# Optimization experiments

Hardware: AMD Instinct MI355X
Metric: run time of the kernel (lower is better)

The kernel has to match this reference:

```python
import jax, jax.numpy as jnp
import numpy as np

B, T, D_MODEL, N_HEADS, N_KV = 2, 2048, 1024, 16, 4
HEAD = D_MODEL // N_HEADS  # 64
NEG_INF = -1e9


def sine_table(features, length):
    # standard RoPE frequency table: theta_i = 10000^(2i/d)
    fraction = jnp.arange(0, features, 2, dtype=jnp.float32) / features
    timescale = 10000.0 ** fraction  # (features/2,)
    sinusoid = jnp.arange(length, dtype=jnp.float32)[:, None] / timescale[None, :]
    sinusoid = jnp.concatenate([sinusoid, sinusoid], axis=-1)  # (L, features)
    return jnp.sin(sinusoid), jnp.cos(sinusoid)


def rotate_half(x):
    x1, x2 = jnp.split(x, 2, axis=-1)
    return jnp.concatenate([-x2, x1], axis=-1)


def apply_rope(x, sin, cos):
    # x: (B, H, T, D); sin/cos: (L, D)
    t = x.shape[-2]
    return x * cos[:t][None, None] + rotate_half(x) * sin[:t][None, None]


def setup_inputs() -> dict:
    key = jax.random.key(0)
    k1, k2, k3, k4 = jax.random.split(key, 4)
    return {
        'q': jax.random.normal(k1, (B, T, D_MODEL), dtype=jnp.float32),
        'k': jax.random.normal(k2, (B, T, N_KV * HEAD), dtype=jnp.float32),
        'v': jax.random.normal(k3, (B, T, N_KV * HEAD), dtype=jnp.float32),
        'w_out': jax.random.normal(k4, (D_MODEL, D_MODEL), dtype=jnp.float32) * 0.02,
    }


def reference(q, k, v, w_out):
    Bq, Tq, C = q.shape
    head = C // N_HEADS
    # split heads: q -> (B, n_heads, T, head); k/v -> (B, n_kv, T, head)
    qh = q.reshape(Bq, Tq, N_HEADS, head).transpose(0, 2, 1, 3)
    kh = k.reshape(Bq, Tq, N_KV, head).transpose(0, 2, 1, 3)
    vh = v.reshape(Bq, Tq, N_KV, head).transpose(0, 2, 1, 3)
    # inline RoPE on q and k
    sin, cos = sine_table(head, Tq)
    qh = apply_rope(qh, sin, cos)
    kh = apply_rope(kh, sin, cos)
    # GQA repeat of kv heads to match q heads
    rep = N_HEADS // N_KV
    kh = jnp.repeat(kh, rep, axis=1)
    vh = jnp.repeat(vh, rep, axis=1)
    # manual scaled-dot-product attention with causal masking (full T^2 logits)
    logits = jnp.einsum('bhqd,bhkd->bhqk', qh, kh) / jnp.sqrt(jnp.float32(head))
    causal = jnp.tril(jnp.ones((Tq, Tq), dtype=jnp.float32))
    logits = jnp.where(causal == 0, NEG_INF, logits)
    attn = jax.nn.softmax(logits, axis=-1)
    out = jnp.einsum('bhqk,bhkd->bhqd', attn, vh)
    out = out.transpose(0, 2, 1, 3).reshape(Bq, Tq, C)
    return out @ w_out
```

## Files before the change

kernel.cpp:

```cpp
#include <hip/hip_runtime.h>
#include <math.h>

#define T_SEQ 2048
#define NH    16
#define NKV   4

typedef __attribute__((ext_vector_type(8)))  _Float16 f16x8;
typedef __attribute__((ext_vector_type(4)))  _Float16 f16x4;
typedef __attribute__((ext_vector_type(2)))  __fp16   fp16x2b;
typedef __attribute__((ext_vector_type(4)))  float    f32x4;

#if __has_builtin(__builtin_amdgcn_exp2f)
#define EXP2F(x) __builtin_amdgcn_exp2f(x)
#else
#define EXP2F(x) exp2f(x)
#endif

#define QSCALE 0.18033688011112042f

__global__ __launch_bounds__(256) void prep_kernel(const float* __restrict__ k,
                                                   const float* __restrict__ v,
                                                   const float* __restrict__ w,
                                                   float2* __restrict__ tb,
                                                   _Float16* __restrict__ Kr,
                                                   _Float16* __restrict__ Vt,
                                                   _Float16* __restrict__ Wt)
{
    __shared__ _Float16 L[64 * 72];
    const int bx = blockIdx.x;
    if (bx < 256) {
        int idx = bx * 256 + threadIdx.x;
        int i = idx & 31, t = idx >> 5;
        float inv = __expf((float)i * (-9.210340371976184f / 32.0f));
        float ang = (float)t * inv;
        tb[idx] = make_float2(cosf(ang), sinf(ang));
    } else if (bx < 512) {
        int idx = (bx - 256) * 256 + threadIdx.x;
        int i   = idx & 31;
        int t   = idx >> 5;
        float inv = __expf((float)i * (-9.210340371976184f / 32.0f));
        float ang = (float)t * inv;
        float sn = sinf(ang), cs = cosf(ang);
        #pragma unroll
        for (int bk = 0; bk < 8; ++bk) {
            const float* src = k + ((size_t)(bk >> 2) * T_SEQ + t) * 256 + (bk & 3) * 64 + i;
            float x1 = src[0], x2 = src[32];
            _Float16* dst = Kr + ((size_t)bk * T_SEQ + t) * 64 + i;
            dst[0]  = (_Float16)(x1 * cs - x2 * sn);
            dst[32] = (_Float16)(x2 * cs + x1 * sn);
        }
    } else if (bx < 768) {
        const int id = bx - 512;
        const int t0 = (id & 31) * 64, bk = id >> 5;
        const int b = bk >> 2, kh = bk & 3;
        const int rr = threadIdx.x >> 2, pp = threadIdx.x & 3;
        const float* src = v + ((size_t)(b * T_SEQ + t0 + rr)) * 256 + kh * 64 + pp * 16;
        f32x4 s0 = *(const f32x4*)(src), s1 = *(const f32x4*)(src + 4);
        f32x4 s2 = *(const f32x4*)(src + 8), s3 = *(const f32x4*)(src + 12);
        _Float16* lp = &L[rr * 72 + pp * 16];
        #pragma unroll
        for (int j = 0; j < 4; ++j) { lp[j] = (_Float16)s0[j]; lp[4+j] = (_Float16)s1[j];
                                      lp[8+j] = (_Float16)s2[j]; lp[12+j] = (_Float16)s3[j]; }
        __syncthreads();
        f16x8 w0, w1;
        #pragma unroll
        for (int j = 0; j < 8; ++j) w0[j] = L[(pp * 16 + j) * 72 + rr];
        #pragma unroll
        for (int j = 0; j < 8; ++j) w1[j] = L[(pp * 16 + 8 + j) * 72 + rr];
        _Float16* dst = Vt + ((size_t)bk * 64 + rr) * T_SEQ + t0 + pp * 16;
        *(f16x8*)dst = w0; *(f16x8*)(dst + 8) = w1;
    } else {
        const int id = bx - 768;
        const int k0 = (id & 15) * 64, n0 = (id >> 4) * 64;
        const int rr = threadIdx.x >> 2, pp = threadIdx.x & 3;
        const float* src = w + (size_t)(k0 + rr) * 1024 + n0 + pp * 16;
        f32x4 s0 = *(const f32x4*)(src), s1 = *(const f32x4*)(src + 4);
        f32x4 s2 = *(const f32x4*)(src + 8), s3 = *(const f32x4*)(src + 12);
        _Float16* lp = &L[rr * 72 + pp * 16];
        #pragma unroll
        for (int j = 0; j < 4; ++j) { lp[j] = (_Float16)s0[j]; lp[4+j] = (_Float16)s1[j];
                                      lp[8+j] = (_Float16)s2[j]; lp[12+j] = (_Float16)s3[j]; }
        __syncthreads();
        f16x8 w0, w1;
        #pragma unroll
        for (int j = 0; j < 8; ++j) w0[j] = L[(pp * 16 + j) * 72 + rr];
        #pragma unroll
        for (int j = 0; j < 8; ++j) w1[j] = L[(pp * 16 + 8 + j) * 72 + rr];
        _Float16* dst = Wt + (size_t)(n0 + rr) * 1024 + k0 + pp * 16;
        *(f16x8*)dst = w0; *(f16x8*)(dst + 8) = w1;
    }
}


__global__ __launch_bounds__(256) void attn_kernel(const float* __restrict__ q,
                                                   const float2* __restrict__ tb,
                                                   const _Float16* __restrict__ Kr,
                                                   const _Float16* __restrict__ Vt,
                                                   _Float16* __restrict__ AO)
{
    __shared__ _Float16 smem[16384];

    const int wid  = threadIdx.x >> 6;
    const int lane = threadIdx.x & 63;
    const int bh = blockIdx.x & 31;
    const int pp = blockIdx.x >> 5;
    const int p  = (pp < 8) ? pp : (23 - pp);
    const int qb0 = p, qb1 = 31 - p;
    const int b = bh >> 4, h = bh & 15;
    const int kh = h >> 2;
    const int bkh = b * NKV + kh;
    const int g = lane >> 4, r = lane & 15;

    const int srow   = wid * 16 + (lane >> 3);
    const int schunk = lane & 7;
    const _Float16* kgbase = Kr + (size_t)bkh * T_SEQ * 64;
    const _Float16* vgbase = Vt + (size_t)bkh * 64 * T_SEQ;
    const int kd0 = srow * 64 + ((schunk ^ (srow & 7)) * 8);
    const int kd1 = kd0 + 8 * 64;

    f16x8 stK0, stK1, stV0, stV1;
    {
        const _Float16* kg = kgbase + (size_t)srow * 64 + schunk * 8;
        stK0 = *(const f16x8*)(kg);
        stK1 = *(const f16x8*)(kg + 8 * 64);
        const _Float16* vg = vgbase + (size_t)srow * T_SEQ + schunk * 8;
        stV0 = *(const f16x8*)(vg);
        stV1 = *(const f16x8*)(vg + 8 * T_SEQ);
    }

    f16x8 qa[2][2];
    #pragma unroll
    for (int tl = 0; tl < 2; ++tl) {
        const int t = (tl ? qb1 : qb0) * 64 + wid * 16 + r;
        const float* qs = q + ((size_t)b * T_SEQ + t) * 1024 + h * 64 + 8 * g;
        const float2* tp = tb + t * 32 + 8 * g;
        #pragma unroll
        for (int j = 0; j < 8; ++j) {
            float x0 = qs[j], x1 = qs[32 + j];
            float2 cs = tp[j];
            qa[tl][0][j] = (_Float16)((x0 * cs.x - x1 * cs.y) * QSCALE);
            qa[tl][1][j] = (_Float16)((x1 * cs.x + x0 * cs.y) * QSCALE);
        }
    }

    *(f16x8*)(&smem[kd0])        = stK0;
    *(f16x8*)(&smem[kd1])        = stK1;
    *(f16x8*)(&smem[8192 + kd0]) = stV0;
    *(f16x8*)(&smem[8192 + kd1]) = stV1;
    __syncthreads();

    f32x4 o[2][4];
    f32x4 o4[2];
    #pragma unroll
    for (int tl = 0; tl < 2; ++tl) {
        #pragma unroll
        for (int db = 0; db < 4; ++db) o[tl][db] = (f32x4){0.f,0.f,0.f,0.f};
        o4[tl] = (f32x4){0.f,0.f,0.f,0.f};
    }
    const f16x4 onesf = {(_Float16)1.f, (_Float16)1.f, (_Float16)1.f, (_Float16)1.f};
    float mrun[2] = {-INFINITY, -INFINITY};
    int cur = 0;

    for (int kvb = 0; kvb <= qb1; ++kvb) {
        const bool hasNext = (kvb < qb1);
        if (hasNext) {
            const int nb = (kvb + 1) * 64;
            const _Float16* kg = kgbase + (size_t)(nb + srow) * 64 + schunk * 8;
            stK0 = *(const f16x8*)(kg);
            stK1 = *(const f16x8*)(kg + 8 * 64);
            const _Float16* vg = vgbase + (size_t)srow * T_SEQ + nb + schunk * 8;
            stV0 = *(const f16x8*)(vg);
            stV1 = *(const f16x8*)(vg + 8 * T_SEQ);
        }
        const bool act0 = (kvb <= qb0);
        const _Float16* ks = smem + cur * 4096;
        const _Float16* vs = smem + 8192 + cur * 4096;

        f32x4 stt[2][4];
        __builtin_amdgcn_s_setprio(1);
        #pragma unroll
        for (int kt = 0; kt < 4; ++kt) {
            f16x8 ka0 = *(const f16x8*)(ks + (kt*16 + r) * 64 + ((g       ^ (r & 7)) * 8));
            f16x8 ka1 = *(const f16x8*)(ks + (kt*16 + r) * 64 + (((4 + g) ^ (r & 7)) * 8));
            f32x4 s1 = {0.f,0.f,0.f,0.f};
            s1 = __builtin_amdgcn_mfma_f32_16x16x32_f16(ka0, qa[1][0], s1, 0, 0, 0);
            s1 = __builtin_amdgcn_mfma_f32_16x16x32_f16(ka1, qa[1][1], s1, 0, 0, 0);
            stt[1][kt] = s1;
            if (act0) {
                f32x4 s0 = {0.f,0.f,0.f,0.f};
                s0 = __builtin_amdgcn_mfma_f32_16x16x32_f16(ka0, qa[0][0], s0, 0, 0, 0);
                s0 = __builtin_amdgcn_mfma_f32_16x16x32_f16(ka1, qa[0][1], s0, 0, 0, 0);
                stt[0][kt] = s0;
            }
        }
        __builtin_amdgcn_s_setprio(0);

        if (kvb == qb0) {
            #pragma unroll
            for (int kt = 0; kt < 4; ++kt)
                #pragma unroll
                for (int j = 0; j < 4; ++j)
                    if (kt*16 + 4*g + j > wid*16 + r) stt[0][kt][j] = -1e9f;
        }
        if (kvb == qb1) {
            #pragma unroll
            for (int kt = 0; kt < 4; ++kt)
                #pragma unroll
                for (int j = 0; j < 4; ++j)
                    if (kt*16 + 4*g + j > wid*16 + r) stt[1][kt][j] = -1e9f;
        }

        f16x4 pf[2][4];
        #pragma unroll
        for (int tl = 0; tl < 2; ++tl) {
            if (tl == 0 && !act0) continue;
            float a0 = fmaxf(fmaxf(stt[tl][0][0], stt[tl][0][1]),
                             fmaxf(stt[tl][0][2], stt[tl][0][3]));
            float a1 = fmaxf(fmaxf(stt[tl][1][0], stt[tl][1][1]),
                             fmaxf(stt[tl][1][2], stt[tl][1][3]));
            float a2 = fmaxf(fmaxf(stt[tl][2][0], stt[tl][2][1]),
                             fmaxf(stt[tl][2][2], stt[tl][2][3]));
            float a3 = fmaxf(fmaxf(stt[tl][3][0], stt[tl][3][1]),
                             fmaxf(stt[tl][3][2], stt[tl][3][3]));
            float pmL = fmaxf(fmaxf(a0, a1), fmaxf(a2, a3));
            if (!__all(pmL <= mrun[tl] + 8.0f)) {
                float pm = fmaxf(pmL, __shfl_xor(pmL, 16));
                pm = fmaxf(pm, __shfl_xor(pm, 32));
                float mn   = fmaxf(mrun[tl], pm);
                float corr = EXP2F(mrun[tl] - mn);
                mrun[tl]   = mn;
                f32x4 cf = { __shfl(corr, 4*g + 0), __shfl(corr, 4*g + 1),
                             __shfl(corr, 4*g + 2), __shfl(corr, 4*g + 3) };
                o[tl][0] *= cf; o[tl][1] *= cf; o[tl][2] *= cf; o[tl][3] *= cf;
                o4[tl]   *= cf;
            }
            #pragma unroll
            for (int kt = 0; kt < 4; ++kt) {
                float p0 = EXP2F(stt[tl][kt][0] - mrun[tl]);
                float p1 = EXP2F(stt[tl][kt][1] - mrun[tl]);
                float p2 = EXP2F(stt[tl][kt][2] - mrun[tl]);
                float p3 = EXP2F(stt[tl][kt][3] - mrun[tl]);
                union { unsigned u[2]; f16x4 v; } pk;
                union { fp16x2b hh; unsigned u; } c0, c1;
                c0.hh = __builtin_amdgcn_cvt_pkrtz(p0, p1);
                c1.hh = __builtin_amdgcn_cvt_pkrtz(p2, p3);
                pk.u[0] = c0.u; pk.u[1] = c1.u;
                pf[tl][kt] = pk.v;
            }
        }

        __builtin_amdgcn_s_setprio(1);
        #pragma unroll
        for (int kt = 0; kt < 4; ++kt) {
            const int vc = ((2*kt + (g >> 1)) ^ (r & 7)) * 8 + (g & 1) * 4;
            f16x4 v0 = *(const f16x4*)(vs + (0*16 + r) * 64 + vc);
            f16x4 v1 = *(const f16x4*)(vs + (1*16 + r) * 64 + vc);
            f16x4 v2 = *(const f16x4*)(vs + (2*16 + r) * 64 + vc);
            f16x4 v3 = *(const f16x4*)(vs + (3*16 + r) * 64 + vc);
            o[1][0] = __builtin_amdgcn_mfma_f32_16x16x16f16(pf[1][kt], v0, o[1][0], 0, 0, 0);
            o[1][1] = __builtin_amdgcn_mfma_f32_16x16x16f16(pf[1][kt], v1, o[1][1], 0, 0, 0);
            o[1][2] = __builtin_amdgcn_mfma_f32_16x16x16f16(pf[1][kt], v2, o[1][2], 0, 0, 0);
            o[1][3] = __builtin_amdgcn_mfma_f32_16x16x16f16(pf[1][kt], v3, o[1][3], 0, 0, 0);
            o4[1]   = __builtin_amdgcn_mfma_f32_16x16x16f16(pf[1][kt], onesf, o4[1], 0, 0, 0);
            if (act0) {
                o[0][0] = __builtin_amdgcn_mfma_f32_16x16x16f16(pf[0][kt], v0, o[0][0], 0, 0, 0);
                o[0][1] = __builtin_amdgcn_mfma_f32_16x16x16f16(pf[0][kt], v1, o[0][1], 0, 0, 0);
                o[0][2] = __builtin_amdgcn_mfma_f32_16x16x16f16(pf[0][kt], v2, o[0][2], 0, 0, 0);
                o[0][3] = __builtin_amdgcn_mfma_f32_16x16x16f16(pf[0][kt], v3, o[0][3], 0, 0, 0);
                o4[0]   = __builtin_amdgcn_mfma_f32_16x16x16f16(pf[0][kt], onesf, o4[0], 0, 0, 0);
            }
        }
        __builtin_amdgcn_s_setprio(0);

        if (hasNext) {
            _Float16* kw = smem + (cur ^ 1) * 4096;
            _Float16* vw = smem + 8192 + (cur ^ 1) * 4096;
            *(f16x8*)(&kw[kd0]) = stK0;
            *(f16x8*)(&kw[kd1]) = stK1;
            *(f16x8*)(&vw[kd0]) = stV0;
            *(f16x8*)(&vw[kd1]) = stV1;
            cur ^= 1;
        }
        __syncthreads();
    }

    #pragma unroll
    for (int tl = 0; tl < 2; ++tl) {
        f32x4 li;
        #pragma unroll
        for (int j = 0; j < 4; ++j) li[j] = 1.0f / o4[tl][j];
        _Float16* Os = smem + tl * 4608;
        #pragma unroll
        for (int db = 0; db < 4; ++db) {
            f32x4 ov = o[tl][db] * li;
            #pragma unroll
            for (int j = 0; j < 4; ++j)
                Os[(wid*16 + 4*g + j) * 72 + db*16 + r] = (_Float16)ov[j];
        }
    }
    __syncthreads();
    {
        const int row = threadIdx.x >> 2, part = threadIdx.x & 3;
        #pragma unroll
        for (int tl = 0; tl < 2; ++tl) {
            const int qb = tl ? qb1 : qb0;
            const _Float16* src = smem + tl * 4608 + row * 72 + part * 16;
            _Float16* dst = AO + ((size_t)b * T_SEQ + qb * 64 + row) * 1024 + h * 64 + part * 16;
            *(f16x8*)dst       = *(const f16x8*)src;
            *(f16x8*)(dst + 8) = *(const f16x8*)(src + 8);
        }
    }
}


#define AST 40
__global__ __launch_bounds__(256) void gemm_kernel(const _Float16* __restrict__ A,
                                                   const _Float16* __restrict__ Bt,
                                                   float* __restrict__ C)
{
    __shared__ _Float16 As[2][128 * AST];
    __shared__ _Float16 Bs[2][64 * AST];
    const int tid  = threadIdx.x;
    const int by   = blockIdx.x & 31;
    const int bx   = blockIdx.x >> 5;
    const int lane = tid & 63;
    const int wid  = tid >> 6;
    const int g = lane >> 4, r = lane & 15;
    const int wm = wid >> 1, wn = wid & 1;

    f32x4 acc[4][2];
    #pragma unroll
    for (int i = 0; i < 4; ++i)
        #pragma unroll
        for (int j = 0; j < 2; ++j) acc[i][j] = (f32x4){0.f,0.f,0.f,0.f};

    const int c0 = tid, c1 = tid + 256;
    const size_t a0off = (size_t)(by*128 + (c0 >> 2)) * 1024 + (c0 & 3) * 8;
    const size_t a1off = (size_t)(by*128 + (c1 >> 2)) * 1024 + (c1 & 3) * 8;
    const size_t b0off = (size_t)(bx*64  + (c0 >> 2)) * 1024 + (c0 & 3) * 8;
    const int ad0 = (c0 >> 2) * AST + (c0 & 3) * 8;
    const int ad1 = (c1 >> 2) * AST + (c1 & 3) * 8;

    f16x8 a0 = *(const f16x8*)(A  + a0off);
    f16x8 a1 = *(const f16x8*)(A  + a1off);
    f16x8 b0 = *(const f16x8*)(Bt + b0off);
    *(f16x8*)(&As[0][ad0]) = a0;
    *(f16x8*)(&As[0][ad1]) = a1;
    *(f16x8*)(&Bs[0][ad0]) = b0;
    __syncthreads();
    int cur = 0;

    for (int kt = 0; kt < 32; ++kt) {
        if (kt < 31) {
            a0 = *(const f16x8*)(A  + a0off + (kt+1) * 32);
            a1 = *(const f16x8*)(A  + a1off + (kt+1) * 32);
            b0 = *(const f16x8*)(Bt + b0off + (kt+1) * 32);
        }
        f16x8 af[4], bfv[2];
        #pragma unroll
        for (int mi = 0; mi < 4; ++mi)
            af[mi] = *(const f16x8*)(&As[cur][(wm*64 + mi*16 + r) * AST + 8 * g]);
        #pragma unroll
        for (int ni = 0; ni < 2; ++ni)
            bfv[ni] = *(const f16x8*)(&Bs[cur][(wn*32 + ni*16 + r) * AST + 8 * g]);
        __builtin_amdgcn_s_setprio(1);
        #pragma unroll
        for (int mi = 0; mi < 4; ++mi)
            #pragma unroll
            for (int ni = 0; ni < 2; ++ni)
                acc[mi][ni] = __builtin_amdgcn_mfma_f32_16x16x32_f16(
                                  af[mi], bfv[ni], acc[mi][ni], 0, 0, 0);
        __builtin_amdgcn_s_setprio(0);
        if (kt < 31) {
            *(f16x8*)(&As[cur ^ 1][ad0]) = a0;
            *(f16x8*)(&As[cur ^ 1][ad1]) = a1;
            *(f16x8*)(&Bs[cur ^ 1][ad0]) = b0;
            cur ^= 1;
        }
        __syncthreads();
    }
    #pragma unroll
    for (int mi = 0; mi < 4; ++mi)
        #pragma unroll
        for (int ni = 0; ni < 2; ++ni)
            #pragma unroll
            for (int j = 0; j < 4; ++j)
                C[(size_t)(by*128 + wm*64 + mi*16 + 4*g + j) * 1024
                  + bx*64 + wn*32 + ni*16 + r] = acc[mi][ni][j];
}


extern "C" void kernel_launch(void* const* d_in, const int* in_sizes, int n_in,
                              void* d_out, int out_size, void* d_ws, size_t ws_size,
                              hipStream_t stream) {
    const float* q = (const float*)d_in[0];
    const float* k = (const float*)d_in[1];
    const float* v = (const float*)d_in[2];
    const float* w = (const float*)d_in[3];
    float* out = (float*)d_out;

    char* ws = (char*)d_ws;
    float2*   tb = (float2*)(ws);
    _Float16* Kr = (_Float16*)(ws + ((size_t)1 << 20));
    _Float16* Vt = (_Float16*)(ws + ((size_t)3 << 20));
    _Float16* Wt = (_Float16*)(ws + ((size_t)5 << 20));
    _Float16* AO = (_Float16*)(ws + ((size_t)7 << 20));

    hipLaunchKernelGGL(prep_kernel,  dim3(1024), dim3(256), 0, stream, k, v, w, tb, Kr, Vt, Wt);
    hipLaunchKernelGGL(attn_kernel,  dim3(512),  dim3(256), 0, stream, q, tb, Kr, Vt, AO);
    hipLaunchKernelGGL(gemm_kernel,  dim3(512),  dim3(256), 0, stream, AO, Wt, out);
}
```

Before: 74.46 us.

## Deepen output-projection GEMM global prefetch to two stages with lighter LDS barrier

The output-projection GEMM now prefetches global tiles two k-steps ahead, using two register sets that alternate across an unrolled pair of iterations, so global load latency gets more time to be hidden. The __syncthreads is replaced by a custom barrier that waits only on lgkmcnt and is fenced by sched_barriers, so the wait no longer covers outstanding global loads. This raises register pressure and constrains the compiler's scheduling across the barrier.

```diff
diff --git a/kernel.cpp b/kernel.cpp
--- a/kernel.cpp
+++ b/kernel.cpp
@@ -17,6 +17,14 @@
 #endif
 
 #define QSCALE 0.18033688011112042f
+
+#define LDS_BARRIER()                                        \
+    do {                                                     \
+        __builtin_amdgcn_sched_barrier(0);                   \
+        asm volatile("s_waitcnt lgkmcnt(0)" ::: "memory");   \
+        __builtin_amdgcn_s_barrier();                        \
+        __builtin_amdgcn_sched_barrier(0);                   \
+    } while (0)
 
 __global__ __launch_bounds__(256) void prep_kernel(const float* __restrict__ k,
                                                    const float* __restrict__ v,
@@ -341,21 +349,27 @@
     const int ad0 = (c0 >> 2) * AST + (c0 & 3) * 8;
     const int ad1 = (c1 >> 2) * AST + (c1 & 3) * 8;
 
-    f16x8 a0 = *(const f16x8*)(A  + a0off);
-    f16x8 a1 = *(const f16x8*)(A  + a1off);
-    f16x8 b0 = *(const f16x8*)(Bt + b0off);
-    *(f16x8*)(&As[0][ad0]) = a0;
-    *(f16x8*)(&As[0][ad1]) = a1;
-    *(f16x8*)(&Bs[0][ad0]) = b0;
+    f16x8 pA0 = *(const f16x8*)(A  + a0off);
+    f16x8 pA1 = *(const f16x8*)(A  + a1off);
+    f16x8 pB0 = *(const f16x8*)(Bt + b0off);
+    *(f16x8*)(&As[0][ad0]) = pA0;
+    *(f16x8*)(&As[0][ad1]) = pA1;
+    *(f16x8*)(&Bs[0][ad0]) = pB0;
+    f16x8 sA0B = *(const f16x8*)(A  + a0off + 32);
+    f16x8 sA1B = *(const f16x8*)(A  + a1off + 32);
+    f16x8 sB0B = *(const f16x8*)(Bt + b0off + 32);
+    f16x8 sA0A, sA1A, sB0A;
     __syncthreads();
-    int cur = 0;
-
-    for (int kt = 0; kt < 32; ++kt) {
-        if (kt < 31) {
-            a0 = *(const f16x8*)(A  + a0off + (kt+1) * 32);
-            a1 = *(const f16x8*)(A  + a1off + (kt+1) * 32);
-            b0 = *(const f16x8*)(Bt + b0off + (kt+1) * 32);
-        }
+
+    auto iter_body = [&](int kt,
+                         f16x8& iA0, f16x8& iA1, f16x8& iB0,
+                         f16x8& oA0, f16x8& oA1, f16x8& oB0) {
+        if (kt + 2 < 32) {
+            iA0 = *(const f16x8*)(A  + a0off + (kt + 2) * 32);
+            iA1 = *(const f16x8*)(A  + a1off + (kt + 2) * 32);
+            iB0 = *(const f16x8*)(Bt + b0off + (kt + 2) * 32);
+        }
+        const int cur = kt & 1;
         f16x8 af[4], bfv[2];
         #pragma unroll
         for (int mi = 0; mi < 4; ++mi)
@@ -371,14 +385,20 @@
                 acc[mi][ni] = __builtin_amdgcn_mfma_f32_16x16x32_f16(
                                   af[mi], bfv[ni], acc[mi][ni], 0, 0, 0);
         __builtin_amdgcn_s_setprio(0);
-        if (kt < 31) {
-            *(f16x8*)(&As[cur ^ 1][ad0]) = a0;
-            *(f16x8*)(&As[cur ^ 1][ad1]) = a1;
-            *(f16x8*)(&Bs[cur ^ 1][ad0]) = b0;
-            cur ^= 1;
-        }
-        __syncthreads();
-    }
+        if (kt + 1 < 32) {
+            *(f16x8*)(&As[cur ^ 1][ad0]) = oA0;
+            *(f16x8*)(&As[cur ^ 1][ad1]) = oA1;
+            *(f16x8*)(&Bs[cur ^ 1][ad0]) = oB0;
+        }
+        LDS_BARRIER();
+    };
+
+    #pragma unroll 2
+    for (int kt = 0; kt < 32; kt += 2) {
+        iter_body(kt,     sA0A, sA1A, sB0A, sA0B, sA1B, sB0B);
+        iter_body(kt + 1, sA0B, sA1B, sB0B, sA0A, sA1A, sB0A);
+    }
+
     #pragma unroll
     for (int mi = 0; mi < 4; ++mi)
         #pragma unroll
```

Result: faster. 72.59 us (-2.5%).
